# Optimization experiments

Hardware: AMD Instinct MI355X
Metric: run time of the kernel (lower is better)

## Reference

```python
import jax, jax.numpy as jnp
import numpy as np

NUM_NODES = 50000
FEAT_DIM = 64
HIDDEN = 128
OUT_DIM = 128
NUM_EDGES = 640000


def setup_inputs() -> dict:
    key = jax.random.key(0)
    ks = jax.random.split(key, 8)
    edge_index = jax.random.randint(ks[0], (2, NUM_EDGES), 0, NUM_NODES, dtype=jnp.int32)
    emb = jax.random.normal(ks[1], (NUM_NODES, FEAT_DIM), dtype=jnp.float32) * 0.1
    # SAGEConv: lin_l (aggregated neighbors, with bias) and lin_r (root, no bias)
    s1 = 1.0 / np.sqrt(FEAT_DIM)
    W1l = jax.random.uniform(ks[2], (HIDDEN, FEAT_DIM), jnp.float32, -s1, s1)
    b1l = jnp.zeros((HIDDEN,), jnp.float32)
    W1r = jax.random.uniform(ks[3], (HIDDEN, FEAT_DIM), jnp.float32, -s1, s1)
    s2 = 1.0 / np.sqrt(HIDDEN)
    W2l = jax.random.uniform(ks[4], (OUT_DIM, HIDDEN), jnp.float32, -s2, s2)
    b2l = jnp.zeros((OUT_DIM,), jnp.float32)
    W2r = jax.random.uniform(ks[5], (OUT_DIM, HIDDEN), jnp.float32, -s2, s2)
    return {"edge_index": edge_index, "emb": emb, "W1l": W1l, "b1l": b1l,
            "W1r": W1r, "W2l": W2l, "b2l": b2l, "W2r": W2r}


def _sage_conv(x, src, dst, Wl, bl, Wr):
    # mean-aggregate source features at target nodes, then two linear paths
    msg = x[src]                                   # [E, d]
    agg = jax.ops.segment_sum(msg, dst, num_segments=NUM_NODES)
    deg = jax.ops.segment_sum(jnp.ones((src.shape[0],), x.dtype), dst,
                              num_segments=NUM_NODES)
    mean = agg / jnp.maximum(deg, 1.0)[:, None]    # [N, d]
    return mean @ Wl.T + bl + x @ Wr.T             # [N, out]


def reference(edge_index, emb, W1l, b1l, W1r, W2l, b2l, W2r):
    src, dst = edge_index[0], edge_index[1]
    h = jax.nn.relu(_sage_conv(emb, src, dst, W1l, b1l, W1r))
    return _sage_conv(h, src, dst, W2l, b2l, W2r)
```

## Files before the change

kernel.cpp:

```cpp
#include <hip/hip_runtime.h>

#define N_NODES 50000
#define FEAT    64
#define HID     128
#define N_EDGES 640000
#define NB      196
#define GCAP    64

typedef __attribute__((ext_vector_type(8))) short bf16x8;
typedef __attribute__((ext_vector_type(4))) float f32x4;

static __device__ __forceinline__ unsigned short f2bf(float f) {
    unsigned u = __float_as_uint(f);
    u = u + 0x7fffu + ((u >> 16) & 1u);
    return (unsigned short)(u >> 16);
}

__global__ void cvt_all_kernel(const float* __restrict__ emb,
                               const float* __restrict__ W1l, const float* __restrict__ W1r,
                               const float* __restrict__ W2l, const float* __restrict__ W2r,
                               unsigned short* __restrict__ emb_bf,
                               unsigned short* __restrict__ Wbf) {
    int id = blockIdx.x * blockDim.x + threadIdx.x;
    if (id < N_NODES * FEAT) {
        emb_bf[id] = f2bf(emb[id]);
    }
    int w = id - N_NODES * FEAT;
    if (w >= 0 && w < 49152) {
        float v;
        if (w < 8192)       v = W1l[w];
        else if (w < 16384) v = W1r[w - 8192];
        else if (w < 32768) v = W2l[w - 16384];
        else                v = W2r[w - 32768];
        Wbf[w] = f2bf(v);
    }
}

__global__ void hist_kernel(const int* __restrict__ dst, int* __restrict__ count) {
    int e = blockIdx.x * blockDim.x + threadIdx.x;
    if (e < N_EDGES) atomicAdd(&count[dst[e]], 1);
}

__global__ __launch_bounds__(256) void scan1_kernel(const int* __restrict__ count,
                                                    int* __restrict__ offset,
                                                    int* __restrict__ bsum,
                                                    int* __restrict__ dhist) {
    __shared__ int tmp[256];
    __shared__ int lh[64];
    int t = threadIdx.x;
    int i = blockIdx.x * 256 + t;
    if (t < 64) lh[t] = 0;
    int v = (i < N_NODES) ? count[i] : 0;
    tmp[t] = v;
    __syncthreads();
    if (i < N_NODES) atomicAdd(&lh[v < 63 ? v : 63], 1);
    for (int off = 1; off < 256; off <<= 1) {
        int add = (t >= off) ? tmp[t - off] : 0;
        __syncthreads();
        tmp[t] += add;
        __syncthreads();
    }
    if (i < N_NODES) offset[i] = tmp[t] - v;
    if (t == 255) bsum[blockIdx.x] = tmp[255];
    if (t < 64 && lh[t] > 0) atomicAdd(&dhist[t], lh[t]);
}

__global__ __launch_bounds__(256) void scan2_kernel(const int* __restrict__ bsum,
                                                    int* __restrict__ boff,
                                                    const int* __restrict__ dhist,
                                                    int* __restrict__ dstart) {
    __shared__ int tmp[256];
    int t = threadIdx.x;
    const int* in  = (blockIdx.x == 0) ? bsum : dhist;
    int*       out = (blockIdx.x == 0) ? boff : dstart;
    int cnt        = (blockIdx.x == 0) ? NB   : 64;
    int v = (t < cnt) ? in[t] : 0;
    tmp[t] = v;
    __syncthreads();
    for (int off = 1; off < 256; off <<= 1) {
        int add = (t >= off) ? tmp[t - off] : 0;
        __syncthreads();
        tmp[t] += add;
        __syncthreads();
    }
    if (t < cnt) out[t] = tmp[t] - v;
}

__global__ void scan3_kernel(int* __restrict__ offset, const int* __restrict__ boff) {
    int i = blockIdx.x * 256 + threadIdx.x;
    if (i < N_NODES) offset[i] += boff[blockIdx.x];
    if (i == 0) offset[N_NODES] = N_EDGES;
}

__global__ void fill_kernel(const int* __restrict__ src, const int* __restrict__ dst,
                            const int* __restrict__ offset, int* __restrict__ cursor,
                            int* __restrict__ esrc) {
    int e = blockIdx.x * blockDim.x + threadIdx.x;
    if (e >= N_EDGES) return;
    int d = dst[e];
    int slot = atomicAdd(&cursor[d], 1);
    esrc[offset[d] + slot] = src[e];
}

__global__ __launch_bounds__(256) void permute_kernel(
        const int* __restrict__ count, const int* __restrict__ dstart,
        int* __restrict__ dcur, int* __restrict__ perm) {
    __shared__ int lbin[64];
    __shared__ int lbase[64];
    int t = threadIdx.x;
    int i = blockIdx.x * 256 + t;
    if (t < 64) lbin[t] = 0;
    __syncthreads();
    int d = 0, slot = 0;
    if (i < N_NODES) {
        int c = count[i];
        d = c < 63 ? c : 63;
        slot = atomicAdd(&lbin[d], 1);
    }
    __syncthreads();
    if (t < 64 && lbin[t] > 0) lbase[t] = atomicAdd(&dcur[t], lbin[t]);
    __syncthreads();
    if (i < N_NODES) perm[dstart[d] + lbase[d] + slot] = i;
}

__global__ __launch_bounds__(256) void gather1_kernel(
        const float4* __restrict__ emb4, const int* __restrict__ offset,
        const int* __restrict__ esrc, const int* __restrict__ perm,
        uint4* __restrict__ mean1_u4) {
    __shared__ int sidx[4][8][GCAP];
    int t = threadIdx.x, wave = t >> 6, lane = t & 63;
    int sub = lane >> 3, fl = lane & 7;
    int widx = blockIdx.x * 32 + wave * 8 + sub;
    bool valid = widx < N_NODES;
    int n = 0, beg = 0, deg = 0;
    if (valid) { n = perm[widx]; beg = offset[n]; deg = offset[n + 1] - beg; }
    bool fast = deg <= GCAP;
    if (valid && fast) {
        for (int j = fl; j < deg; j += 8) sidx[wave][sub][j] = esrc[beg + j];
    }
    __syncthreads();
    float a[8] = {0.f,0.f,0.f,0.f,0.f,0.f,0.f,0.f};
    if (valid) {
        if (fast) {
            int i = 0;
            for (; i + 4 <= deg; i += 4) {
                int s0 = sidx[wave][sub][i+0], s1 = sidx[wave][sub][i+1];
                int s2 = sidx[wave][sub][i+2], s3 = sidx[wave][sub][i+3];
                float4 v0 = emb4[s0*8+fl], v1 = emb4[s1*8+fl];
                float4 v2 = emb4[s2*8+fl], v3 = emb4[s3*8+fl];
                #define ACC1(v) { \
                    unsigned ux=__float_as_uint((v).x),uy=__float_as_uint((v).y); \
                    unsigned uz=__float_as_uint((v).z),uw=__float_as_uint((v).w); \
                    a[0]+=__uint_as_float(ux<<16); a[1]+=__uint_as_float(ux&0xffff0000u); \
                    a[2]+=__uint_as_float(uy<<16); a[3]+=__uint_as_float(uy&0xffff0000u); \
                    a[4]+=__uint_as_float(uz<<16); a[5]+=__uint_as_float(uz&0xffff0000u); \
                    a[6]+=__uint_as_float(uw<<16); a[7]+=__uint_as_float(uw&0xffff0000u); }
                ACC1(v0) ACC1(v1) ACC1(v2) ACC1(v3)
            }
            for (; i < deg; ++i) { float4 v = emb4[sidx[wave][sub][i]*8+fl]; ACC1(v) }
        } else {
            for (int i = 0; i < deg; ++i) { float4 v = emb4[esrc[beg+i]*8+fl]; ACC1(v) }
        }
        float dinv = 1.0f / fmaxf((float)deg, 1.0f);
        uint4 o;
        o.x = ((unsigned)f2bf(a[1]*dinv) << 16) | (unsigned)f2bf(a[0]*dinv);
        o.y = ((unsigned)f2bf(a[3]*dinv) << 16) | (unsigned)f2bf(a[2]*dinv);
        o.z = ((unsigned)f2bf(a[5]*dinv) << 16) | (unsigned)f2bf(a[4]*dinv);
        o.w = ((unsigned)f2bf(a[7]*dinv) << 16) | (unsigned)f2bf(a[6]*dinv);
        mean1_u4[n*8 + fl] = o;
    }
}

__global__ __launch_bounds__(256) void gather2_kernel(
        const float4* __restrict__ h4, const int* __restrict__ offset,
        const int* __restrict__ esrc, const int* __restrict__ perm,
        uint4* __restrict__ mean2_u4) {
    __shared__ int sidx[4][4][GCAP];
    int t = threadIdx.x, wave = t >> 6, lane = t & 63;
    int sub = lane >> 4, fl = lane & 15;
    int widx = blockIdx.x * 16 + wave * 4 + sub;
    bool valid = widx < N_NODES;
    int n = 0, beg = 0, deg = 0;
    if (valid) { n = perm[widx]; beg = offset[n]; deg = offset[n + 1] - beg; }
    bool fast = deg <= GCAP;
    if (valid && fast) {
        for (int j = fl; j < deg; j += 16) sidx[wave][sub][j] = esrc[beg + j];
    }
    __syncthreads();
    float a[8] = {0.f,0.f,0.f,0.f,0.f,0.f,0.f,0.f};
    if (valid) {
        if (fast) {
            int i = 0;
            for (; i + 4 <= deg; i += 4) {
                int s0 = sidx[wave][sub][i+0], s1 = sidx[wave][sub][i+1];
                int s2 = sidx[wave][sub][i+2], s3 = sidx[wave][sub][i+3];
                float4 v0 = h4[s0*16+fl], v1 = h4[s1*16+fl];
                float4 v2 = h4[s2*16+fl], v3 = h4[s3*16+fl];
                ACC1(v0) ACC1(v1) ACC1(v2) ACC1(v3)
            }
            for (; i < deg; ++i) { float4 v = h4[sidx[wave][sub][i]*16+fl]; ACC1(v) }
        } else {
            for (int i = 0; i < deg; ++i) { float4 v = h4[esrc[beg+i]*16+fl]; ACC1(v) }
        }
        float dinv = 1.0f / fmaxf((float)deg, 1.0f);
        uint4 o;
        o.x = ((unsigned)f2bf(a[1]*dinv) << 16) | (unsigned)f2bf(a[0]*dinv);
        o.y = ((unsigned)f2bf(a[3]*dinv) << 16) | (unsigned)f2bf(a[2]*dinv);
        o.z = ((unsigned)f2bf(a[5]*dinv) << 16) | (unsigned)f2bf(a[4]*dinv);
        o.w = ((unsigned)f2bf(a[7]*dinv) << 16) | (unsigned)f2bf(a[6]*dinv);
        mean2_u4[n*16 + fl] = o;
    }
}

__global__ __launch_bounds__(256) void gemm1_kernel(
        const short* __restrict__ mean1, const short* __restrict__ embb,
        const short* __restrict__ Wl, const short* __restrict__ Wr,
        const float* __restrict__ bias, unsigned short* __restrict__ hout) {
    int wid = blockIdx.x * 4 + (threadIdx.x >> 6);
    if (wid >= N_NODES / 16) return;
    int lane = threadIdx.x & 63;
    int col = lane & 15, quad = lane >> 4;
    int m0 = wid * 16;
    f32x4 acc[8];
    #pragma unroll
    for (int nt = 0; nt < 8; ++nt) acc[nt] = (f32x4){0.f,0.f,0.f,0.f};
    #pragma unroll
    for (int kb = 0; kb < FEAT; kb += 32) {
        bf16x8 a = *(const bf16x8*)(mean1 + (m0 + col) * FEAT + kb + quad * 8);
        #pragma unroll
        for (int nt = 0; nt < 8; ++nt) {
            bf16x8 b = *(const bf16x8*)(Wl + (nt * 16 + col) * FEAT + kb + quad * 8);
            acc[nt] = __builtin_amdgcn_mfma_f32_16x16x32_bf16(a, b, acc[nt], 0, 0, 0);
        }
    }
    #pragma unroll
    for (int kb = 0; kb < FEAT; kb += 32) {
        bf16x8 a = *(const bf16x8*)(embb + (m0 + col) * FEAT + kb + quad * 8);
        #pragma unroll
        for (int nt = 0; nt < 8; ++nt) {
            bf16x8 b = *(const bf16x8*)(Wr + (nt * 16 + col) * FEAT + kb + quad * 8);
            acc[nt] = __builtin_amdgcn_mfma_f32_16x16x32_bf16(a, b, acc[nt], 0, 0, 0);
        }
    }
    #pragma unroll
    for (int nt = 0; nt < 8; ++nt) {
        float bv = bias[nt * 16 + col];
        #pragma unroll
        for (int r = 0; r < 4; ++r) {
            float v = fmaxf(acc[nt][r] + bv, 0.f);
            hout[(m0 + quad * 4 + r) * HID + nt * 16 + col] = f2bf(v);
        }
    }
}

__global__ __launch_bounds__(256) void gemm2_kernel(
        const short* __restrict__ mean2, const short* __restrict__ hbf,
        const short* __restrict__ Wl, const short* __restrict__ Wr,
        const float* __restrict__ bias, float* __restrict__ out) {
    int wid = blockIdx.x * 4 + (threadIdx.x >> 6);
    if (wid >= N_NODES / 16) return;
    int lane = threadIdx.x & 63;
    int col = lane & 15, quad = lane >> 4;
    int m0 = wid * 16;
    f32x4 acc[8];
    #pragma unroll
    for (int nt = 0; nt < 8; ++nt) acc[nt] = (f32x4){0.f,0.f,0.f,0.f};
    #pragma unroll
    for (int kb = 0; kb < HID; kb += 32) {
        bf16x8 a = *(const bf16x8*)(mean2 + (m0 + col) * HID + kb + quad * 8);
        #pragma unroll
        for (int nt = 0; nt < 8; ++nt) {
            bf16x8 b = *(const bf16x8*)(Wl + (nt * 16 + col) * HID + kb + quad * 8);
            acc[nt] = __builtin_amdgcn_mfma_f32_16x16x32_bf16(a, b, acc[nt], 0, 0, 0);
        }
    }
    #pragma unroll
    for (int kb = 0; kb < HID; kb += 32) {
        bf16x8 a = *(const bf16x8*)(hbf + (m0 + col) * HID + kb + quad * 8);
        #pragma unroll
        for (int nt = 0; nt < 8; ++nt) {
            bf16x8 b = *(const bf16x8*)(Wr + (nt * 16 + col) * HID + kb + quad * 8);
            acc[nt] = __builtin_amdgcn_mfma_f32_16x16x32_bf16(a, b, acc[nt], 0, 0, 0);
        }
    }
    #pragma unroll
    for (int nt = 0; nt < 8; ++nt) {
        float bv = bias[nt * 16 + col];
        #pragma unroll
        for (int r = 0; r < 4; ++r) {
            out[(m0 + quad * 4 + r) * HID + nt * 16 + col] = acc[nt][r] + bv;
        }
    }
}

extern "C" void kernel_launch(void* const* d_in, const int* in_sizes, int n_in,
                              void* d_out, int out_size, void* d_ws, size_t ws_size,
                              hipStream_t stream) {
    const int*   edge_index = (const int*)d_in[0];
    const float* emb        = (const float*)d_in[1];
    const float* W1l        = (const float*)d_in[2];
    const float* b1l        = (const float*)d_in[3];
    const float* W1r        = (const float*)d_in[4];
    const float* W2l        = (const float*)d_in[5];
    const float* b2l        = (const float*)d_in[6];
    const float* W2r        = (const float*)d_in[7];
    float* out = (float*)d_out;

    const int* src = edge_index;
    const int* dst = edge_index + N_EDGES;

    int* iws    = (int*)d_ws;
    int* offset = iws;
    int* count  = iws + 50004;
    int* cursor = iws + 100004;
    int* dhist  = iws + 150004;
    int* dcur   = iws + 150068;
    int* bsum   = iws + 150132;
    int* boff   = iws + 150388;
    int* dstart = iws + 150644;
    int* perm   = iws + 150712;
    int* esrc   = iws + 200712;
    unsigned short* W1l_bf = (unsigned short*)(iws + 840712);
    unsigned short* W1r_bf = (unsigned short*)(iws + 844808);
    unsigned short* W2l_bf = (unsigned short*)(iws + 848904);
    unsigned short* W2r_bf = (unsigned short*)(iws + 857096);
    unsigned short* Wbf    = W1l_bf;
    unsigned short* emb_bf = (unsigned short*)(iws + 865288);
    unsigned short* mean1  = (unsigned short*)(iws + 2465288);
    unsigned short* hbf    = (unsigned short*)(iws + 4065288);
    unsigned short* mean2  = (unsigned short*)(iws + 7265288);

    hipMemsetAsync(count, 0, (size_t)(150132 - 50004) * sizeof(int), stream);

    cvt_all_kernel<<<(N_NODES * FEAT + 49152 + 255) / 256, 256, 0, stream>>>(
        emb, W1l, W1r, W2l, W2r, emb_bf, Wbf);

    hist_kernel<<<(N_EDGES + 255) / 256, 256, 0, stream>>>(dst, count);
    scan1_kernel<<<NB, 256, 0, stream>>>(count, offset, bsum, dhist);
    scan2_kernel<<<2, 256, 0, stream>>>(bsum, boff, dhist, dstart);
    scan3_kernel<<<NB, 256, 0, stream>>>(offset, boff);
    fill_kernel<<<(N_EDGES + 255) / 256, 256, 0, stream>>>(src, dst, offset, cursor, esrc);
    permute_kernel<<<NB, 256, 0, stream>>>(count, dstart, dcur, perm);

    gather1_kernel<<<(N_NODES + 31) / 32, 256, 0, stream>>>(
        (const float4*)emb_bf, offset, esrc, perm, (uint4*)mean1);
    gemm1_kernel<<<(N_NODES / 16 + 3) / 4, 256, 0, stream>>>(
        (const short*)mean1, (const short*)emb_bf,
        (const short*)W1l_bf, (const short*)W1r_bf, b1l, hbf);
    gather2_kernel<<<(N_NODES + 15) / 16, 256, 0, stream>>>(
        (const float4*)hbf, offset, esrc, perm, (uint4*)mean2);
    gemm2_kernel<<<(N_NODES / 16 + 3) / 4, 256, 0, stream>>>(
        (const short*)mean2, (const short*)hbf,
        (const short*)W2l_bf, (const short*)W2r_bf, b2l, out);
}
```

Measured before the change: 264.3 us.

## Fuse CSR build and bf16 conversion into one persistent kernel with grid barriers

Replaces the memset, conversion, histogram, three scan kernels, fill and permute launches with a single 196-block persistent kernel that separates phases using an atomic software grid barrier. This removes several kernel launch gaps and the separate memset. The fused kernel also converts emb two elements at a time. Separately, the gather kernels get an 8-way unrolled neighbor loop to keep more loads in flight. The grid barrier depends on all 196 blocks being resident at once, and each phase now runs on only about 50K threads via grid-stride loops.

After: 322.2 us. 1.22x slower.

```diff
diff --git a/kernel.cpp b/kernel.cpp
--- a/kernel.cpp
+++ b/kernel.cpp
@@ -4,7 +4,8 @@
 #define FEAT    64
 #define HID     128
 #define N_EDGES 640000
-#define NB      196
+#define NBLK    196
+#define GSZ     (NBLK * 256)
 #define GCAP    64
 
 typedef __attribute__((ext_vector_type(8))) short bf16x8;
@@ -16,111 +17,114 @@
     return (unsigned short)(u >> 16);
 }
 
-__global__ void cvt_all_kernel(const float* __restrict__ emb,
-                               const float* __restrict__ W1l, const float* __restrict__ W1r,
-                               const float* __restrict__ W2l, const float* __restrict__ W2r,
-                               unsigned short* __restrict__ emb_bf,
-                               unsigned short* __restrict__ Wbf) {
-    int id = blockIdx.x * blockDim.x + threadIdx.x;
-    if (id < N_NODES * FEAT) {
-        emb_bf[id] = f2bf(emb[id]);
-    }
-    int w = id - N_NODES * FEAT;
-    if (w >= 0 && w < 49152) {
-        float v;
-        if (w < 8192)       v = W1l[w];
-        else if (w < 16384) v = W1r[w - 8192];
-        else if (w < 32768) v = W2l[w - 16384];
-        else                v = W2r[w - 32768];
-        Wbf[w] = f2bf(v);
-    }
-}
-
-__global__ void hist_kernel(const int* __restrict__ dst, int* __restrict__ count) {
-    int e = blockIdx.x * blockDim.x + threadIdx.x;
-    if (e < N_EDGES) atomicAdd(&count[dst[e]], 1);
-}
-
-__global__ __launch_bounds__(256) void scan1_kernel(const int* __restrict__ count,
-                                                    int* __restrict__ offset,
-                                                    int* __restrict__ bsum,
-                                                    int* __restrict__ dhist) {
+static __device__ __forceinline__ void gridbar(int* bar, int gen) {
+    __syncthreads();
+    if (threadIdx.x == 0) {
+        __threadfence();
+        int arrived = atomicAdd(&bar[0], 1);
+        if (arrived == NBLK - 1) {
+            atomicExch(&bar[0], 0);
+            __threadfence();
+            atomicExch(&bar[1], gen);
+        } else {
+            while (atomicAdd(&bar[1], 0) < gen) __builtin_amdgcn_s_sleep(2);
+        }
+        __threadfence();
+    }
+    __syncthreads();
+}
+
+__global__ __launch_bounds__(256) void csr_kernel(
+        const int* __restrict__ src, const int* __restrict__ dst,
+        const float* __restrict__ emb,
+        const float* __restrict__ W1l, const float* __restrict__ W1r,
+        const float* __restrict__ W2l, const float* __restrict__ W2r,
+        int* count, int* offset, int* cursor, int* dhist, int* dcur,
+        int* bsum, int* boff, int* dstart, int* perm, int* esrc,
+        unsigned* emb_bf_u, unsigned* Wbf_u, int* bar) {
     __shared__ int tmp[256];
     __shared__ int lh[64];
+    __shared__ int lb2[64];
     int t = threadIdx.x;
-    int i = blockIdx.x * 256 + t;
-    if (t < 64) lh[t] = 0;
-    int v = (i < N_NODES) ? count[i] : 0;
-    tmp[t] = v;
-    __syncthreads();
-    if (i < N_NODES) atomicAdd(&lh[v < 63 ? v : 63], 1);
-    for (int off = 1; off < 256; off <<= 1) {
-        int add = (t >= off) ? tmp[t - off] : 0;
-        __syncthreads();
-        tmp[t] += add;
-        __syncthreads();
-    }
-    if (i < N_NODES) offset[i] = tmp[t] - v;
-    if (t == 255) bsum[blockIdx.x] = tmp[255];
-    if (t < 64 && lh[t] > 0) atomicAdd(&dhist[t], lh[t]);
-}
-
-__global__ __launch_bounds__(256) void scan2_kernel(const int* __restrict__ bsum,
-                                                    int* __restrict__ boff,
-                                                    const int* __restrict__ dhist,
-                                                    int* __restrict__ dstart) {
-    __shared__ int tmp[256];
-    int t = threadIdx.x;
-    const int* in  = (blockIdx.x == 0) ? bsum : dhist;
-    int*       out = (blockIdx.x == 0) ? boff : dstart;
-    int cnt        = (blockIdx.x == 0) ? NB   : 64;
-    int v = (t < cnt) ? in[t] : 0;
-    tmp[t] = v;
-    __syncthreads();
-    for (int off = 1; off < 256; off <<= 1) {
-        int add = (t >= off) ? tmp[t - off] : 0;
-        __syncthreads();
-        tmp[t] += add;
-        __syncthreads();
-    }
-    if (t < cnt) out[t] = tmp[t] - v;
-}
-
-__global__ void scan3_kernel(int* __restrict__ offset, const int* __restrict__ boff) {
-    int i = blockIdx.x * 256 + threadIdx.x;
-    if (i < N_NODES) offset[i] += boff[blockIdx.x];
-    if (i == 0) offset[N_NODES] = N_EDGES;
-}
-
-__global__ void fill_kernel(const int* __restrict__ src, const int* __restrict__ dst,
-                            const int* __restrict__ offset, int* __restrict__ cursor,
-                            int* __restrict__ esrc) {
-    int e = blockIdx.x * blockDim.x + threadIdx.x;
-    if (e >= N_EDGES) return;
-    int d = dst[e];
-    int slot = atomicAdd(&cursor[d], 1);
-    esrc[offset[d] + slot] = src[e];
-}
-
-__global__ __launch_bounds__(256) void permute_kernel(
-        const int* __restrict__ count, const int* __restrict__ dstart,
-        int* __restrict__ dcur, int* __restrict__ perm) {
-    __shared__ int lbin[64];
-    __shared__ int lbase[64];
-    int t = threadIdx.x;
-    int i = blockIdx.x * 256 + t;
-    if (t < 64) lbin[t] = 0;
-    __syncthreads();
-    int d = 0, slot = 0;
-    if (i < N_NODES) {
-        int c = count[i];
-        d = c < 63 ? c : 63;
-        slot = atomicAdd(&lbin[d], 1);
-    }
-    __syncthreads();
-    if (t < 64 && lbin[t] > 0) lbase[t] = atomicAdd(&dcur[t], lbin[t]);
-    __syncthreads();
-    if (i < N_NODES) perm[dstart[d] + lbase[d] + slot] = i;
+    int gtid = blockIdx.x * 256 + t;
+
+    for (int i = gtid; i < 100128; i += GSZ) count[i] = 0;
+    for (int i = gtid; i < N_NODES * FEAT / 2; i += GSZ) {
+        float2 v = ((const float2*)emb)[i];
+        emb_bf_u[i] = ((unsigned)f2bf(v.y) << 16) | (unsigned)f2bf(v.x);
+    }
+    for (int p = gtid; p < 24576; p += GSZ) {
+        int w = p * 2;
+        float lo, hi;
+        if (w < 8192)       { lo = W1l[w];         hi = W1l[w + 1]; }
+        else if (w < 16384) { lo = W1r[w - 8192];  hi = W1r[w - 8191]; }
+        else if (w < 32768) { lo = W2l[w - 16384]; hi = W2l[w - 16383]; }
+        else                { lo = W2r[w - 32768]; hi = W2r[w - 32767]; }
+        Wbf_u[p] = ((unsigned)f2bf(hi) << 16) | (unsigned)f2bf(lo);
+    }
+    gridbar(bar, 1);
+
+    for (int e = gtid; e < N_EDGES; e += GSZ) atomicAdd(&count[dst[e]], 1);
+    gridbar(bar, 2);
+
+    {
+        if (t < 64) lh[t] = 0;
+        int v = (gtid < N_NODES) ? count[gtid] : 0;
+        tmp[t] = v;
+        __syncthreads();
+        if (gtid < N_NODES) atomicAdd(&lh[v < 63 ? v : 63], 1);
+        for (int off = 1; off < 256; off <<= 1) {
+            int add = (t >= off) ? tmp[t - off] : 0;
+            __syncthreads();
+            tmp[t] += add;
+            __syncthreads();
+        }
+        if (gtid < N_NODES) offset[gtid] = tmp[t] - v;
+        if (t == 255) bsum[blockIdx.x] = tmp[255];
+        if (t < 64 && lh[t] > 0) atomicAdd(&dhist[t], lh[t]);
+    }
+    gridbar(bar, 3);
+
+    if (blockIdx.x < 2) {
+        const int* in  = (blockIdx.x == 0) ? bsum : dhist;
+        int*       out = (blockIdx.x == 0) ? boff : dstart;
+        int cnt        = (blockIdx.x == 0) ? NBLK : 64;
+        int v = (t < cnt) ? in[t] : 0;
+        tmp[t] = v;
+        __syncthreads();
+        for (int off = 1; off < 256; off <<= 1) {
+            int add = (t >= off) ? tmp[t - off] : 0;
+            __syncthreads();
+            tmp[t] += add;
+            __syncthreads();
+        }
+        if (t < cnt) out[t] = tmp[t] - v;
+    }
+    gridbar(bar, 4);
+
+    if (gtid < N_NODES) offset[gtid] += boff[blockIdx.x];
+    if (gtid == 0) offset[N_NODES] = N_EDGES;
+    gridbar(bar, 5);
+
+    for (int e = gtid; e < N_EDGES; e += GSZ) {
+        int d = dst[e];
+        int slot = atomicAdd(&cursor[d], 1);
+        esrc[offset[d] + slot] = src[e];
+    }
+    {
+        if (t < 64) lh[t] = 0;
+        __syncthreads();
+        int d = 0, slot = 0;
+        if (gtid < N_NODES) {
+            int c = count[gtid];
+            d = c < 63 ? c : 63;
+            slot = atomicAdd(&lh[d], 1);
+        }
+        __syncthreads();
+        if (t < 64 && lh[t] > 0) lb2[t] = atomicAdd(&dcur[t], lh[t]);
+        __syncthreads();
+        if (gtid < N_NODES) perm[dstart[d] + lb2[d] + slot] = gtid;
+    }
 }
 
 __global__ __launch_bounds__(256) void gather1_kernel(
@@ -141,20 +145,32 @@
     __syncthreads();
     float a[8] = {0.f,0.f,0.f,0.f,0.f,0.f,0.f,0.f};
     if (valid) {
+        #define ACC1(v) { \
+            unsigned ux=__float_as_uint((v).x),uy=__float_as_uint((v).y); \
+            unsigned uz=__float_as_uint((v).z),uw=__float_as_uint((v).w); \
+            a[0]+=__uint_as_float(ux<<16); a[1]+=__uint_as_float(ux&0xffff0000u); \
+            a[2]+=__uint_as_float(uy<<16); a[3]+=__uint_as_float(uy&0xffff0000u); \
+            a[4]+=__uint_as_float(uz<<16); a[5]+=__uint_as_float(uz&0xffff0000u); \
+            a[6]+=__uint_as_float(uw<<16); a[7]+=__uint_as_float(uw&0xffff0000u); }
         if (fast) {
             int i = 0;
+            for (; i + 8 <= deg; i += 8) {
+                float4 v0 = emb4[sidx[wave][sub][i+0]*8+fl];
+                float4 v1 = emb4[sidx[wave][sub][i+1]*8+fl];
+                float4 v2 = emb4[sidx[wave][sub][i+2]*8+fl];
+                float4 v3 = emb4[sidx[wave][sub][i+3]*8+fl];
+                float4 v4 = emb4[sidx[wave][sub][i+4]*8+fl];
+                float4 v5 = emb4[sidx[wave][sub][i+5]*8+fl];
+                float4 v6 = emb4[sidx[wave][sub][i+6]*8+fl];
+                float4 v7 = emb4[sidx[wave][sub][i+7]*8+fl];
+                ACC1(v0) ACC1(v1) ACC1(v2) ACC1(v3)
+                ACC1(v4) ACC1(v5) ACC1(v6) ACC1(v7)
+            }
             for (; i + 4 <= deg; i += 4) {
-                int s0 = sidx[wave][sub][i+0], s1 = sidx[wave][sub][i+1];
-                int s2 = sidx[wave][sub][i+2], s3 = sidx[wave][sub][i+3];
-                float4 v0 = emb4[s0*8+fl], v1 = emb4[s1*8+fl];
-                float4 v2 = emb4[s2*8+fl], v3 = emb4[s3*8+fl];
-                #define ACC1(v) { \
-                    unsigned ux=__float_as_uint((v).x),uy=__float_as_uint((v).y); \
-                    unsigned uz=__float_as_uint((v).z),uw=__float_as_uint((v).w); \
-                    a[0]+=__uint_as_float(ux<<16); a[1]+=__uint_as_float(ux&0xffff0000u); \
-                    a[2]+=__uint_as_float(uy<<16); a[3]+=__uint_as_float(uy&0xffff0000u); \
-                    a[4]+=__uint_as_float(uz<<16); a[5]+=__uint_as_float(uz&0xffff0000u); \
-                    a[6]+=__uint_as_float(uw<<16); a[7]+=__uint_as_float(uw&0xffff0000u); }
+                float4 v0 = emb4[sidx[wave][sub][i+0]*8+fl];
+                float4 v1 = emb4[sidx[wave][sub][i+1]*8+fl];
+                float4 v2 = emb4[sidx[wave][sub][i+2]*8+fl];
+                float4 v3 = emb4[sidx[wave][sub][i+3]*8+fl];
                 ACC1(v0) ACC1(v1) ACC1(v2) ACC1(v3)
             }
             for (; i < deg; ++i) { float4 v = emb4[sidx[wave][sub][i]*8+fl]; ACC1(v) }
@@ -191,11 +207,23 @@
     if (valid) {
         if (fast) {
             int i = 0;
+            for (; i + 8 <= deg; i += 8) {
+                float4 v0 = h4[sidx[wave][sub][i+0]*16+fl];
+                float4 v1 = h4[sidx[wave][sub][i+1]*16+fl];
+                float4 v2 = h4[sidx[wave][sub][i+2]*16+fl];
+                float4 v3 = h4[sidx[wave][sub][i+3]*16+fl];
+                float4 v4 = h4[sidx[wave][sub][i+4]*16+fl];
+                float4 v5 = h4[sidx[wave][sub][i+5]*16+fl];
+                float4 v6 = h4[sidx[wave][sub][i+6]*16+fl];
+                float4 v7 = h4[sidx[wave][sub][i+7]*16+fl];
+                ACC1(v0) ACC1(v1) ACC1(v2) ACC1(v3)
+                ACC1(v4) ACC1(v5) ACC1(v6) ACC1(v7)
+            }
             for (; i + 4 <= deg; i += 4) {
-                int s0 = sidx[wave][sub][i+0], s1 = sidx[wave][sub][i+1];
-                int s2 = sidx[wave][sub][i+2], s3 = sidx[wave][sub][i+3];
-                float4 v0 = h4[s0*16+fl], v1 = h4[s1*16+fl];
-                float4 v2 = h4[s2*16+fl], v3 = h4[s3*16+fl];
+                float4 v0 = h4[sidx[wave][sub][i+0]*16+fl];
+                float4 v1 = h4[sidx[wave][sub][i+1]*16+fl];
+                float4 v2 = h4[sidx[wave][sub][i+2]*16+fl];
+                float4 v3 = h4[sidx[wave][sub][i+3]*16+fl];
                 ACC1(v0) ACC1(v1) ACC1(v2) ACC1(v3)
             }
             for (; i < deg; ++i) { float4 v = h4[sidx[wave][sub][i]*16+fl]; ACC1(v) }
@@ -318,6 +346,7 @@
     int* bsum   = iws + 150132;
     int* boff   = iws + 150388;
     int* dstart = iws + 150644;
+    int* bar    = iws + 150708;
     int* perm   = iws + 150712;
     int* esrc   = iws + 200712;
     unsigned short* W1l_bf = (unsigned short*)(iws + 840712);
@@ -330,17 +359,12 @@
     unsigned short* hbf    = (unsigned short*)(iws + 4065288);
     unsigned short* mean2  = (unsigned short*)(iws + 7265288);
 
-    hipMemsetAsync(count, 0, (size_t)(150132 - 50004) * sizeof(int), stream);
-
-    cvt_all_kernel<<<(N_NODES * FEAT + 49152 + 255) / 256, 256, 0, stream>>>(
-        emb, W1l, W1r, W2l, W2r, emb_bf, Wbf);
-
-    hist_kernel<<<(N_EDGES + 255) / 256, 256, 0, stream>>>(dst, count);
-    scan1_kernel<<<NB, 256, 0, stream>>>(count, offset, bsum, dhist);
-    scan2_kernel<<<2, 256, 0, stream>>>(bsum, boff, dhist, dstart);
-    scan3_kernel<<<NB, 256, 0, stream>>>(offset, boff);
-    fill_kernel<<<(N_EDGES + 255) / 256, 256, 0, stream>>>(src, dst, offset, cursor, esrc);
-    permute_kernel<<<NB, 256, 0, stream>>>(count, dstart, dcur, perm);
+    hipMemsetAsync(bar, 0, 2 * sizeof(int), stream);
+
+    csr_kernel<<<NBLK, 256, 0, stream>>>(
+        src, dst, emb, W1l, W1r, W2l, W2r,
+        count, offset, cursor, dhist, dcur, bsum, boff, dstart, perm, esrc,
+        (unsigned*)emb_bf, (unsigned*)Wbf, bar);
 
     gather1_kernel<<<(N_NODES + 31) / 32, 256, 0, stream>>>(
         (const float4*)emb_bf, offset, esrc, perm, (uint4*)mean1);
```
